# Optimization experiments

Hardware: AMD Instinct MI355X
Metric: run time of the kernel (lower is better)

Reference implementation:

```python
import jax, jax.numpy as jnp
import numpy as np

B = 131072
HIDDEN = [512, 512, 512, 512]
BETA = 20.0  # Softplus(beta=20)


def setup_inputs() -> dict:
    key = jax.random.key(0)
    dims = [3] + HIDDEN + [2]  # in_dim=3, out = div_mat_dim + 1 = 2
    n_layers = len(dims) - 1
    ks = jax.random.split(key, 1 + 2 * n_layers)
    d = {"tx": jax.random.normal(ks[0], (B, 3), dtype=jnp.float32)}
    for i, (din, dout) in enumerate(zip(dims[:-1], dims[1:])):
        lim = 1.0 / np.sqrt(din)  # torch nn.Linear default init
        d[f"W{i}"] = jax.random.uniform(ks[1 + 2 * i], (dout, din), jnp.float32, -lim, lim)
        d[f"b{i}"] = jax.random.uniform(ks[2 + 2 * i], (dout,), jnp.float32, -lim, lim)
    return d


def reference(tx, W0, b0, W1, b1, W2, b2, W3, b3, W4, b4):
    params = [(W0, b0), (W1, b1), (W2, b2), (W3, b3), (W4, b4)]

    def mlp(x):
        h = x
        for W, b in params[:-1]:
            # torch Softplus(beta=20): softplus(beta*x)/beta
            h = jax.nn.softplus(BETA * (h @ W.T + b)) / BETA
        W, b = params[-1]
        return h @ W.T + b  # [..., 2]: (stream fn s, pressure p)

    # div_A_matrix builds the 2x2 antisymmetric matrix A with A[0,1]=s, A[1,0]=-s.
    # vmap(jacrev(div_A_matrix)) then einsum('...ii') over the spatial cols (x,y)
    # reduces exactly to u = (ds/dy, -ds/dx). Per-sample grads of s are obtained
    # with one vectorized backward pass (samples are independent).
    g = jax.grad(lambda t: mlp(t)[:, 0].sum())(tx)  # [B, 3] cols = (t, x, y)
    u = jnp.stack([g[:, 2], -g[:, 1]], axis=1)      # [B, 2]
    p = mlp(tx)[:, -1:]                              # [B, 1]
    # torch .squeeze(0) is a no-op for B > 1
    return jnp.concatenate([u, p], axis=1)           # [B, 3]
```

## Files before the change

### kernel.cpp

```cpp
#include <hip/hip_runtime.h>

typedef _Float16 f16;
typedef __attribute__((ext_vector_type(8))) _Float16 f16x8;
typedef __attribute__((ext_vector_type(4))) float f32x4;

#define BT   131072
#define DD   512
#define TM   32
#define NBLK (BT / TM)

__device__ __forceinline__ void stA(char* tb, int row, int colbyte, float v) {
    *(f16*)(tb + row * 1024 + (colbyte ^ ((row & 7) << 4))) = (f16)v;
}
__device__ __forceinline__ f16x8 ldA8(const char* tb, int row, int kbyte) {
    return *(const f16x8*)(tb + row * 1024 + (kbyte ^ ((row & 7) << 4)));
}
__device__ __forceinline__ float ldh(const char* tb, int row, int colbyte) {
    return (float)*(const f16*)(tb + row * 1024 + (colbyte ^ ((row & 7) << 4)));
}

__device__ __forceinline__ f16x8 cvt8(const float* q) {
    float4 u0 = *(const float4*)q;
    float4 u1 = *(const float4*)(q + 4);
    f16x8 r;
    r[0] = (f16)u0.x; r[1] = (f16)u0.y; r[2] = (f16)u0.z; r[3] = (f16)u0.w;
    r[4] = (f16)u1.x; r[5] = (f16)u1.y; r[6] = (f16)u1.z; r[7] = (f16)u1.w;
    return r;
}

__global__ void prep_w(const float* __restrict__ W1, const float* __restrict__ W2,
                       const float* __restrict__ W3, f16* __restrict__ wp) {
    int tid = blockIdx.x * 256 + threadIdx.x;
    if (tid >= 6 * 16 * 32 * 64) return;
    int lane = tid & 63;
    int frag = tid >> 6;
    int nsub = frag & 31;
    int sk   = (frag >> 5) & 15;
    int l    = frag >> 9;
    int lw   = l - (l >= 3 ? 3 : 0);
    const float* W = (lw == 0) ? W1 : (lw == 1) ? W2 : W3;
    int n = nsub * 16 + (lane & 15);
    int k = sk * 32 + (lane >> 4) * 8;
    f16x8 o;
    if (l < 3) {
        const float* p = W + (size_t)n * DD + k;
        #pragma unroll
        for (int j = 0; j < 8; ++j) o[j] = (f16)p[j];
    } else {
        const float* p = W + (size_t)k * DD + n;
        #pragma unroll
        for (int j = 0; j < 8; ++j) o[j] = (f16)p[j * DD];
    }
    ((f16x8*)wp)[tid] = o;
}

#define MFMA1(A, B, C) __builtin_amdgcn_mfma_f32_16x16x32_f16(A, B, C, 0, 0, 0)

#define MFMA_SK2(TB, skc, Q0, Q1, Q2, Q3)                                      \
    { f16x8 aA = ldA8(TB, l15,      (skc) * 64 + g16 * 16);                    \
      f16x8 aB = ldA8(TB, 16 + l15, (skc) * 64 + g16 * 16);                    \
      acc[0][0] = MFMA1(aA, Q0, acc[0][0]); acc[0][1] = MFMA1(aA, Q1, acc[0][1]); \
      acc[0][2] = MFMA1(aA, Q2, acc[0][2]); acc[0][3] = MFMA1(aA, Q3, acc[0][3]); \
      acc[1][0] = MFMA1(aB, Q0, acc[1][0]); acc[1][1] = MFMA1(aB, Q1, acc[1][1]); \
      acc[1][2] = MFMA1(aB, Q2, acc[1][2]); acc[1][3] = MFMA1(aB, Q3, acc[1][3]); }

#define LOADB_P(wS, Q0, Q1, Q2, Q3, skc)                                       \
    { const f16x8* p_ = (wS) + ((size_t)(skc) << 11);                          \
      Q0 = p_[0]; Q1 = p_[64]; Q2 = p_[128]; Q3 = p_[192]; }

template<bool PREP>
__global__ __launch_bounds__(512) void mlp_fused(
    const float* __restrict__ tx,
    const float* __restrict__ W0, const float* __restrict__ b0v,
    const float* __restrict__ W1, const float* __restrict__ b1v,
    const float* __restrict__ W2, const float* __restrict__ b2v,
    const float* __restrict__ W3, const float* __restrict__ b3v,
    const float* __restrict__ W4, const float* __restrict__ b4v,
    const f16* __restrict__ wp, float* __restrict__ out)
{
    __shared__ __align__(16) short abuf_s[4 * 32 * DD];
    __shared__ float txb[TM * 3];
    __shared__ float pbuf[8][32];
    char* ab = (char*)abuf_s;
    char* G  = ab + 3 * 32768;

    const int tid  = threadIdx.x;
    const int lane = tid & 63;
    const int wv   = tid >> 6;
    const int g16  = lane >> 4;
    const int l15  = lane & 15;
    const long s0  = (long)blockIdx.x * TM;

    if (tid < TM * 3) txb[tid] = tx[s0 * 3 + tid];
    __syncthreads();

    {
        int n = tid;
        float w0 = W0[n * 3 + 0], w1 = W0[n * 3 + 1], w2 = W0[n * 3 + 2], bb = b0v[n];
        #pragma unroll 4
        for (int s = 0; s < TM; ++s) {
            float z  = fmaf(w0, txb[s * 3], fmaf(w1, txb[s * 3 + 1], fmaf(w2, txb[s * 3 + 2], bb)));
            float aa = fabsf(z);
            float e  = __expf(-20.f * aa);
            float dd = 1.f + e;
            float h  = fmaxf(z, 0.f) + __logf(dd) * 0.05f;
            stA(ab, s, n * 2, h);
        }
    }
    __syncthreads();

    for (int i = 0; i < 3; ++i) {
        const float* Wl = (i == 0) ? W1 : (i == 1) ? W2 : W3;
        const float* bl = (i == 0) ? b1v : (i == 1) ? b2v : b3v;
        const f16x8* wS = (const f16x8*)wp + (size_t)i * (16 * 32 * 64)
                        + (size_t)(wv * 4) * 64 + lane;
        const char* Tin = ab + i * 32768;

        f32x4 acc[2][4];
        #pragma unroll
        for (int m = 0; m < 2; ++m)
            #pragma unroll
            for (int n = 0; n < 4; ++n)
                acc[m][n] = f32x4{0.f, 0.f, 0.f, 0.f};

        #pragma unroll 2
        for (int sk = 0; sk < 16; ++sk) {
            f16x8 b0, b1, b2, b3;
            if constexpr (PREP) {
                LOADB_P(wS, b0, b1, b2, b3, sk)
            } else {
                const float* q = Wl + (size_t)(wv * 64 + l15) * DD + sk * 32 + g16 * 8;
                b0 = cvt8(q);
                b1 = cvt8(q + 16 * DD);
                b2 = cvt8(q + 32 * DD);
                b3 = cvt8(q + 48 * DD);
            }
            MFMA_SK2(Tin, sk, b0, b1, b2, b3)
        }

        if (i < 2) {
            char* Tout = ab + (i + 1) * 32768;
            #pragma unroll
            for (int m = 0; m < 2; ++m)
                #pragma unroll
                for (int n = 0; n < 4; ++n) {
                    float bias = bl[wv * 64 + n * 16 + l15];
                    int   cb   = (wv * 64 + n * 16 + l15) * 2;
                    #pragma unroll
                    for (int r = 0; r < 4; ++r) {
                        int row = m * 16 + g16 * 4 + r;
                        float z  = acc[m][n][r] + bias;
                        float aa = fabsf(z);
                        float e  = __expf(-20.f * aa);
                        float dd = 1.f + e;
                        float h  = fmaxf(z, 0.f) + __logf(dd) * 0.05f;
                        stA(Tout, row, cb, h);
                    }
                }
        } else {
            #pragma unroll
            for (int m = 0; m < 2; ++m)
                #pragma unroll
                for (int r = 0; r < 4; ++r) {
                    int row = m * 16 + g16 * 4 + r;
                    float pp = 0.f;
                    #pragma unroll
                    for (int n = 0; n < 4; ++n) {
                        int col = wv * 64 + n * 16 + l15;
                        float z  = acc[m][n][r] + bl[col];
                        float aa = fabsf(z);
                        float e  = __expf(-20.f * aa);
                        float dd = 1.f + e;
                        float rd = __builtin_amdgcn_rcpf(dd);
                        float h4 = fmaxf(z, 0.f) + __logf(dd) * 0.05f;
                        float sg = (z > 0.f ? 1.f : e) * rd;
                        pp = fmaf(W4[DD + col], h4, pp);
                        stA(G, row, col * 2, W4[col] * sg);
                    }
                    pp += __shfl_xor(pp, 1);
                    pp += __shfl_xor(pp, 2);
                    pp += __shfl_xor(pp, 4);
                    pp += __shfl_xor(pp, 8);
                    if (l15 == 0) pbuf[wv][row] = pp;
                }
        }
        __syncthreads();
    }

    for (int b = 0; b < 3; ++b) {
        const f16x8* wS = (const f16x8*)wp + (size_t)(5 - b) * (16 * 32 * 64)
                        + (size_t)(wv * 4) * 64 + lane;
        const float* Wb = (b == 0) ? W3 : (b == 1) ? W2 : W1;
        const char* Th = ab + (2 - b) * 32768;

        f32x4 acc[2][4];
        #pragma unroll
        for (int m = 0; m < 2; ++m)
            #pragma unroll
            for (int n = 0; n < 4; ++n)
                acc[m][n] = f32x4{0.f, 0.f, 0.f, 0.f};

        #pragma unroll 2
        for (int sk = 0; sk < 16; ++sk) {
            f16x8 b0, b1, b2, b3;
            if constexpr (PREP) {
                LOADB_P(wS, b0, b1, b2, b3, sk)
            } else {
                const float* q = Wb + (size_t)(sk * 32 + g16 * 8) * DD + wv * 64 + l15;
                f16x8 t0, t1, t2, t3;
                #pragma unroll
                for (int j = 0; j < 8; ++j) {
                    t0[j] = (f16)q[j * DD];
                    t1[j] = (f16)q[j * DD + 16];
                    t2[j] = (f16)q[j * DD + 32];
                    t3[j] = (f16)q[j * DD + 48];
                }
                b0 = t0; b1 = t1; b2 = t2; b3 = t3;
            }
            MFMA_SK2(G, sk, b0, b1, b2, b3)
        }
        __syncthreads();

        #pragma unroll
        for (int m = 0; m < 2; ++m)
            #pragma unroll
            for (int n = 0; n < 4; ++n) {
                int cb = (wv * 64 + n * 16 + l15) * 2;
                #pragma unroll
                for (int r = 0; r < 4; ++r) {
                    int row = m * 16 + g16 * 4 + r;
                    float h  = ldh(Th, row, cb);
                    float sg = 1.f - __expf(-20.f * h);
                    stA(G, row, cb, sg * acc[m][n][r]);
                }
            }
        __syncthreads();
    }

    {
        const int kb = lane * 8;
        float wyr[8], wxr[8];
        #pragma unroll
        for (int j = 0; j < 8; ++j) {
            wyr[j] = W0[(kb + j) * 3 + 2];
            wxr[j] = W0[(kb + j) * 3 + 1];
        }
        float bp = b4v[1];
        #pragma unroll
        for (int ii = 0; ii < 4; ++ii) {
            int s = wv * 4 + ii;
            f16x8 gg = ldA8(G, s, lane * 16);
            float dy = 0.f, dx = 0.f;
            #pragma unroll
            for (int j = 0; j < 8; ++j) {
                dy = fmaf(wyr[j], (float)gg[j], dy);
                dx = fmaf(wxr[j], (float)gg[j], dx);
            }
            #pragma unroll
            for (int mk = 1; mk < 64; mk <<= 1) {
                dy += __shfl_xor(dy, mk);
                dx += __shfl_xor(dx, mk);
            }
            if (lane == 0) {
                float ps = bp;
                #pragma unroll
                for (int w = 0; w < 8; ++w) ps += pbuf[w][s];
                float* o = out + (s0 + s) * 3;
                o[0] = dy;
                o[1] = -dx;
                o[2] = ps;
            }
        }
    }
}

extern "C" void kernel_launch(void* const* d_in, const int* in_sizes, int n_in,
                              void* d_out, int out_size, void* d_ws, size_t ws_size,
                              hipStream_t stream) {
    const float* tx = (const float*)d_in[0];
    const float* W0 = (const float*)d_in[1]; const float* b0 = (const float*)d_in[2];
    const float* W1 = (const float*)d_in[3]; const float* b1 = (const float*)d_in[4];
    const float* W2 = (const float*)d_in[5]; const float* b2 = (const float*)d_in[6];
    const float* W3 = (const float*)d_in[7]; const float* b3 = (const float*)d_in[8];
    const float* W4 = (const float*)d_in[9]; const float* b4 = (const float*)d_in[10];
    float* out = (float*)d_out;

    const size_t need = (size_t)6 * 512 * 512 * sizeof(f16);
    if (ws_size >= need) {
        f16* wp = (f16*)d_ws;
        prep_w<<<(6 * 16 * 32 * 64 + 255) / 256, 256, 0, stream>>>(W1, W2, W3, wp);
        mlp_fused<true><<<NBLK, 512, 0, stream>>>(tx, W0, b0, W1, b1, W2, b2, W3, b3, W4, b4, wp, out);
    } else {
        mlp_fused<false><<<NBLK, 512, 0, stream>>>(tx, W0, b0, W1, b1, W2, b2, W3, b3, W4, b4, nullptr, out);
    }
}
```

Before: 776.3 us.

## Double block size to 1024 threads, halving each wave's output column tile

Raises the workgroup from 8 to 16 waves. Each wave now computes 32 output columns instead of 64 in every forward and backward GEMM, and the layer-0 and final reduction loops are split across the extra waves. The goal is more latency hiding per CU and lower per-wave register pressure while keeping the same 32-sample tile and LDS footprint. The cost is twice as many A-tile LDS reads per unit of MFMA work, since A is reused across only two B fragments, plus more barrier participants.

```diff
diff --git a/kernel.cpp b/kernel.cpp
--- a/kernel.cpp
+++ b/kernel.cpp
@@ -56,20 +56,18 @@
 
 #define MFMA1(A, B, C) __builtin_amdgcn_mfma_f32_16x16x32_f16(A, B, C, 0, 0, 0)
 
-#define MFMA_SK2(TB, skc, Q0, Q1, Q2, Q3)                                      \
+#define MFMA_SK2(TB, skc, Q0, Q1)                                              \
     { f16x8 aA = ldA8(TB, l15,      (skc) * 64 + g16 * 16);                    \
       f16x8 aB = ldA8(TB, 16 + l15, (skc) * 64 + g16 * 16);                    \
       acc[0][0] = MFMA1(aA, Q0, acc[0][0]); acc[0][1] = MFMA1(aA, Q1, acc[0][1]); \
-      acc[0][2] = MFMA1(aA, Q2, acc[0][2]); acc[0][3] = MFMA1(aA, Q3, acc[0][3]); \
-      acc[1][0] = MFMA1(aB, Q0, acc[1][0]); acc[1][1] = MFMA1(aB, Q1, acc[1][1]); \
-      acc[1][2] = MFMA1(aB, Q2, acc[1][2]); acc[1][3] = MFMA1(aB, Q3, acc[1][3]); }
-
-#define LOADB_P(wS, Q0, Q1, Q2, Q3, skc)                                       \
+      acc[1][0] = MFMA1(aB, Q0, acc[1][0]); acc[1][1] = MFMA1(aB, Q1, acc[1][1]); }
+
+#define LOADB_P(wS, Q0, Q1, skc)                                               \
     { const f16x8* p_ = (wS) + ((size_t)(skc) << 11);                          \
-      Q0 = p_[0]; Q1 = p_[64]; Q2 = p_[128]; Q3 = p_[192]; }
+      Q0 = p_[0]; Q1 = p_[64]; }
 
 template<bool PREP>
-__global__ __launch_bounds__(512) void mlp_fused(
+__global__ __launch_bounds__(1024) void mlp_fused(
     const float* __restrict__ tx,
     const float* __restrict__ W0, const float* __restrict__ b0v,
     const float* __restrict__ W1, const float* __restrict__ b1v,
@@ -80,7 +78,7 @@
 {
     __shared__ __align__(16) short abuf_s[4 * 32 * DD];
     __shared__ float txb[TM * 3];
-    __shared__ float pbuf[8][32];
+    __shared__ float pbuf[16][32];
     char* ab = (char*)abuf_s;
     char* G  = ab + 3 * 32768;
 
@@ -95,10 +93,12 @@
     __syncthreads();
 
     {
-        int n = tid;
+        int n  = tid & 511;
+        int sb = (tid >> 9) * 16;
         float w0 = W0[n * 3 + 0], w1 = W0[n * 3 + 1], w2 = W0[n * 3 + 2], bb = b0v[n];
         #pragma unroll 4
-        for (int s = 0; s < TM; ++s) {
+        for (int si = 0; si < 16; ++si) {
+            int s = sb + si;
             float z  = fmaf(w0, txb[s * 3], fmaf(w1, txb[s * 3 + 1], fmaf(w2, txb[s * 3 + 2], bb)));
             float aa = fabsf(z);
             float e  = __expf(-20.f * aa);
@@ -113,29 +113,24 @@
         const float* Wl = (i == 0) ? W1 : (i == 1) ? W2 : W3;
         const float* bl = (i == 0) ? b1v : (i == 1) ? b2v : b3v;
         const f16x8* wS = (const f16x8*)wp + (size_t)i * (16 * 32 * 64)
-                        + (size_t)(wv * 4) * 64 + lane;
+                        + (size_t)(wv * 2) * 64 + lane;
         const char* Tin = ab + i * 32768;
 
-        f32x4 acc[2][4];
-        #pragma unroll
-        for (int m = 0; m < 2; ++m)
-            #pragma unroll
-            for (int n = 0; n < 4; ++n)
-                acc[m][n] = f32x4{0.f, 0.f, 0.f, 0.f};
+        f32x4 acc[2][2];
+        acc[0][0] = f32x4{0.f,0.f,0.f,0.f}; acc[0][1] = f32x4{0.f,0.f,0.f,0.f};
+        acc[1][0] = f32x4{0.f,0.f,0.f,0.f}; acc[1][1] = f32x4{0.f,0.f,0.f,0.f};
 
         #pragma unroll 2
         for (int sk = 0; sk < 16; ++sk) {
-            f16x8 b0, b1, b2, b3;
+            f16x8 b0, b1;
             if constexpr (PREP) {
-                LOADB_P(wS, b0, b1, b2, b3, sk)
+                LOADB_P(wS, b0, b1, sk)
             } else {
-                const float* q = Wl + (size_t)(wv * 64 + l15) * DD + sk * 32 + g16 * 8;
+                const float* q = Wl + (size_t)(wv * 32 + l15) * DD + sk * 32 + g16 * 8;
                 b0 = cvt8(q);
                 b1 = cvt8(q + 16 * DD);
-                b2 = cvt8(q + 32 * DD);
-                b3 = cvt8(q + 48 * DD);
-            }
-            MFMA_SK2(Tin, sk, b0, b1, b2, b3)
+            }
+            MFMA_SK2(Tin, sk, b0, b1)
         }
 
         if (i < 2) {
@@ -143,9 +138,9 @@
             #pragma unroll
             for (int m = 0; m < 2; ++m)
                 #pragma unroll
-                for (int n = 0; n < 4; ++n) {
-                    float bias = bl[wv * 64 + n * 16 + l15];
-                    int   cb   = (wv * 64 + n * 16 + l15) * 2;
+                for (int n = 0; n < 2; ++n) {
+                    float bias = bl[wv * 32 + n * 16 + l15];
+                    int   cb   = (wv * 32 + n * 16 + l15) * 2;
                     #pragma unroll
                     for (int r = 0; r < 4; ++r) {
                         int row = m * 16 + g16 * 4 + r;
@@ -165,8 +160,8 @@
                     int row = m * 16 + g16 * 4 + r;
                     float pp = 0.f;
                     #pragma unroll
-                    for (int n = 0; n < 4; ++n) {
-                        int col = wv * 64 + n * 16 + l15;
+                    for (int n = 0; n < 2; ++n) {
+                        int col = wv * 32 + n * 16 + l15;
                         float z  = acc[m][n][r] + bl[col];
                         float aa = fabsf(z);
                         float e  = __expf(-20.f * aa);
@@ -189,43 +184,38 @@
 
     for (int b = 0; b < 3; ++b) {
         const f16x8* wS = (const f16x8*)wp + (size_t)(5 - b) * (16 * 32 * 64)
-                        + (size_t)(wv * 4) * 64 + lane;
+                        + (size_t)(wv * 2) * 64 + lane;
         const float* Wb = (b == 0) ? W3 : (b == 1) ? W2 : W1;
         const char* Th = ab + (2 - b) * 32768;
 
-        f32x4 acc[2][4];
-        #pragma unroll
-        for (int m = 0; m < 2; ++m)
-            #pragma unroll
-            for (int n = 0; n < 4; ++n)
-                acc[m][n] = f32x4{0.f, 0.f, 0.f, 0.f};
+        f32x4 acc[2][2];
+        acc[0][0] = f32x4{0.f,0.f,0.f,0.f}; acc[0][1] = f32x4{0.f,0.f,0.f,0.f};
+        acc[1][0] = f32x4{0.f,0.f,0.f,0.f}; acc[1][1] = f32x4{0.f,0.f,0.f,0.f};
 
         #pragma unroll 2
         for (int sk = 0; sk < 16; ++sk) {
-            f16x8 b0, b1, b2, b3;
+            f16x8 b0, b1;
             if constexpr (PREP) {
-                LOADB_P(wS, b0, b1, b2, b3, sk)
+                LOADB_P(wS, b0, b1, sk)
             } else {
-                const float* q = Wb + (size_t)(sk * 32 + g16 * 8) * DD + wv * 64 + l15;
-                f16x8 t0, t1, t2, t3;
+                const float* q = Wb + (size_t)(sk * 32 + g16 * 8) * DD + wv * 32 + l15;
+                f16x8 t0, t1;
                 #pragma unroll
                 for (int j = 0; j < 8; ++j) {
                     t0[j] = (f16)q[j * DD];
                     t1[j] = (f16)q[j * DD + 16];
-                    t2[j] = (f16)q[j * DD + 32];
-                    t3[j] = (f16)q[j * DD + 48];
-                }
-                b0 = t0; b1 = t1; b2 = t2; b3 = t3;
-            }
-            MFMA_SK2(G, sk, b0, b1, b2, b3)
+                }
+                b0 = t0; b1 = t1;
+            }
+            MFMA_SK2(G, sk, b0, b1)
         }
         __syncthreads();
 
         #pragma unroll
         for (int m = 0; m < 2; ++m)
             #pragma unroll
-            for (int n = 0; n < 4; ++n) {
-                int cb = (wv * 64 + n * 16 + l15) * 2;
+            for (int n = 0; n < 2; ++n) {
+                int cb = (wv * 32 + n * 16 + l15) * 2;
                 #pragma unroll
                 for (int r = 0; r < 4; ++r) {
                     int row = m * 16 + g16 * 4 + r;
@@ -247,8 +237,8 @@
         }
         float bp = b4v[1];
         #pragma unroll
-        for (int ii = 0; ii < 4; ++ii) {
-            int s = wv * 4 + ii;
+        for (int ii = 0; ii < 2; ++ii) {
+            int s = wv * 2 + ii;
             f16x8 gg = ldA8(G, s, lane * 16);
             float dy = 0.f, dx = 0.f;
             #pragma unroll
@@ -264,7 +254,7 @@
             if (lane == 0) {
                 float ps = bp;
                 #pragma unroll
-                for (int w = 0; w < 8; ++w) ps += pbuf[w][s];
+                for (int w = 0; w < 16; ++w) ps += pbuf[w][s];
                 float* o = out + (s0 + s) * 3;
                 o[0] = dy;
                 o[1] = -dx;
@@ -289,8 +279,8 @@
     if (ws_size >= need) {
         f16* wp = (f16*)d_ws;
         prep_w<<<(6 * 16 * 32 * 64 + 255) / 256, 256, 0, stream>>>(W1, W2, W3, wp);
-        mlp_fused<true><<<NBLK, 512, 0, stream>>>(tx, W0, b0, W1, b1, W2, b2, W3, b3, W4, b4, wp, out);
+        mlp_fused<true><<<NBLK, 1024, 0, stream>>>(tx, W0, b0, W1, b1, W2, b2, W3, b3, W4, b4, wp, out);
     } else {
-        mlp_fused<false><<<NBLK, 512, 0, stream>>>(tx, W0, b0, W1, b1, W2, b2, W3, b3, W4, b4, nullptr, out);
-    }
-}
+        mlp_fused<false><<<NBLK, 1024, 0, stream>>>(tx, W0, b0, W1, b1, W2, b2, W3, b3, W4, b4, nullptr, out);
+    }
+}
```

After: 754.3 us. 2.8% less time.

## Process two 32-row sub-tiles per block to reuse weight loads

Applied to the files above, without the earlier changes.

Doubles the rows per block to 64 by running two 32-row sub-tiles that share each loaded weight fragment, so every B-operand load feeds twice as many MFMAs. The shared-memory plan changes from one buffer per layer to two ping-pong slots per sub-tile. The layer-1 softplus derivatives are kept in registers as f16, and the layer-0 derivative is recomputed from the inputs instead of being read back from stored activations. The cost is more accumulator and register pressure, which may lower occupancy, and half as many blocks in the grid.

```diff
diff --git a/kernel.cpp b/kernel.cpp
--- a/kernel.cpp
+++ b/kernel.cpp
@@ -6,8 +6,8 @@
 
 #define BT   131072
 #define DD   512
-#define TM   32
-#define NBLK (BT / TM)
+#define TMB  64
+#define NBLK (BT / TMB)
 
 __device__ __forceinline__ void stA(char* tb, int row, int colbyte, float v) {
     *(f16*)(tb + row * 1024 + (colbyte ^ ((row & 7) << 4))) = (f16)v;
@@ -56,17 +56,51 @@
 
 #define MFMA1(A, B, C) __builtin_amdgcn_mfma_f32_16x16x32_f16(A, B, C, 0, 0, 0)
 
-#define MFMA_SK2(TB, skc, Q0, Q1, Q2, Q3)                                      \
-    { f16x8 aA = ldA8(TB, l15,      (skc) * 64 + g16 * 16);                    \
-      f16x8 aB = ldA8(TB, 16 + l15, (skc) * 64 + g16 * 16);                    \
-      acc[0][0] = MFMA1(aA, Q0, acc[0][0]); acc[0][1] = MFMA1(aA, Q1, acc[0][1]); \
-      acc[0][2] = MFMA1(aA, Q2, acc[0][2]); acc[0][3] = MFMA1(aA, Q3, acc[0][3]); \
-      acc[1][0] = MFMA1(aB, Q0, acc[1][0]); acc[1][1] = MFMA1(aB, Q1, acc[1][1]); \
-      acc[1][2] = MFMA1(aB, Q2, acc[1][2]); acc[1][3] = MFMA1(aB, Q3, acc[1][3]); }
-
-#define LOADB_P(wS, Q0, Q1, Q2, Q3, skc)                                       \
-    { const f16x8* p_ = (wS) + ((size_t)(skc) << 11);                          \
-      Q0 = p_[0]; Q1 = p_[64]; Q2 = p_[128]; Q3 = p_[192]; }
+#define MFMA_TILE(ACC, SA, skc, Q0, Q1, Q2, Q3)                                \
+    { f16x8 a0_ = ldA8(SA, l15,      (skc) * 64 + g16 * 16);                   \
+      f16x8 a1_ = ldA8(SA, 16 + l15, (skc) * 64 + g16 * 16);                   \
+      ACC[0][0]=MFMA1(a0_,Q0,ACC[0][0]); ACC[0][1]=MFMA1(a0_,Q1,ACC[0][1]);    \
+      ACC[0][2]=MFMA1(a0_,Q2,ACC[0][2]); ACC[0][3]=MFMA1(a0_,Q3,ACC[0][3]);    \
+      ACC[1][0]=MFMA1(a1_,Q0,ACC[1][0]); ACC[1][1]=MFMA1(a1_,Q1,ACC[1][1]);    \
+      ACC[1][2]=MFMA1(a1_,Q2,ACC[1][2]); ACC[1][3]=MFMA1(a1_,Q3,ACC[1][3]); }
+
+#define ZACC(A)                                                                \
+    _Pragma("unroll") for (int m_ = 0; m_ < 2; ++m_)                           \
+    _Pragma("unroll") for (int n_ = 0; n_ < 4; ++n_)                           \
+        A[m_][n_] = f32x4{0.f, 0.f, 0.f, 0.f};
+
+#define KLOOP_P(SEC, SLOT)                                                     \
+  { const f16x8* wS = (const f16x8*)wp + (size_t)(SEC) * (16*32*64)            \
+                    + (size_t)(wv * 4) * 64 + lane;                            \
+    _Pragma("unroll 2")                                                        \
+    for (int sk = 0; sk < 16; ++sk) {                                          \
+      const f16x8* p_ = wS + ((size_t)sk << 11);                               \
+      f16x8 q0 = p_[0], q1 = p_[64], q2 = p_[128], q3 = p_[192];               \
+      MFMA_TILE(acc0, TA0 + (SLOT)*32768, sk, q0, q1, q2, q3)                  \
+      MFMA_TILE(acc1, TA1 + (SLOT)*32768, sk, q0, q1, q2, q3)                  \
+    } }
+
+#define KLOOP_FW(WPTR, SLOT)                                                   \
+  { _Pragma("unroll 2")                                                        \
+    for (int sk = 0; sk < 16; ++sk) {                                          \
+      const float* q_ = WPTR + (size_t)(wv*64 + l15)*DD + sk*32 + g16*8;       \
+      f16x8 q0 = cvt8(q_), q1 = cvt8(q_ + 16*DD);                              \
+      f16x8 q2 = cvt8(q_ + 32*DD), q3 = cvt8(q_ + 48*DD);                      \
+      MFMA_TILE(acc0, TA0 + (SLOT)*32768, sk, q0, q1, q2, q3)                  \
+      MFMA_TILE(acc1, TA1 + (SLOT)*32768, sk, q0, q1, q2, q3)                  \
+    } }
+
+#define KLOOP_BW(WPTR, SLOT)                                                   \
+  { for (int sk = 0; sk < 16; ++sk) {                                          \
+      const float* q_ = WPTR + (size_t)(sk*32 + g16*8)*DD + wv*64 + l15;       \
+      f16x8 t0, t1, t2, t3;                                                    \
+      _Pragma("unroll")                                                        \
+      for (int j = 0; j < 8; ++j) {                                            \
+          t0[j] = (f16)q_[j*DD];      t1[j] = (f16)q_[j*DD + 16];              \
+          t2[j] = (f16)q_[j*DD + 32]; t3[j] = (f16)q_[j*DD + 48]; }            \
+      MFMA_TILE(acc0, TA0 + (SLOT)*32768, sk, t0, t1, t2, t3)                  \
+      MFMA_TILE(acc1, TA1 + (SLOT)*32768, sk, t0, t1, t2, t3)                  \
+    } }
 
 template<bool PREP>
 __global__ __launch_bounds__(512) void mlp_fused(
@@ -79,163 +113,190 @@
     const f16* __restrict__ wp, float* __restrict__ out)
 {
     __shared__ __align__(16) short abuf_s[4 * 32 * DD];
-    __shared__ float txb[TM * 3];
-    __shared__ float pbuf[8][32];
-    char* ab = (char*)abuf_s;
-    char* G  = ab + 3 * 32768;
+    __shared__ float txb[TMB * 3];
+    __shared__ float pbuf[2][8][32];
+    char* ab  = (char*)abuf_s;
+    char* TA0 = ab;
+    char* TA1 = ab + 65536;
 
     const int tid  = threadIdx.x;
     const int lane = tid & 63;
     const int wv   = tid >> 6;
     const int g16  = lane >> 4;
     const int l15  = lane & 15;
-    const long s0  = (long)blockIdx.x * TM;
-
-    if (tid < TM * 3) txb[tid] = tx[s0 * 3 + tid];
+    const long s0g = (long)blockIdx.x * TMB;
+
+    if (tid < TMB * 3) txb[tid] = tx[s0g * 3 + tid];
     __syncthreads();
 
     {
         int n = tid;
-        float w0 = W0[n * 3 + 0], w1 = W0[n * 3 + 1], w2 = W0[n * 3 + 2], bb = b0v[n];
+        float w0 = W0[n*3], w1 = W0[n*3+1], w2 = W0[n*3+2], bb = b0v[n];
         #pragma unroll 4
-        for (int s = 0; s < TM; ++s) {
-            float z  = fmaf(w0, txb[s * 3], fmaf(w1, txb[s * 3 + 1], fmaf(w2, txb[s * 3 + 2], bb)));
+        for (int s = 0; s < TMB; ++s) {
+            float z  = fmaf(w0, txb[s*3], fmaf(w1, txb[s*3+1], fmaf(w2, txb[s*3+2], bb)));
             float aa = fabsf(z);
             float e  = __expf(-20.f * aa);
-            float dd = 1.f + e;
-            float h  = fmaxf(z, 0.f) + __logf(dd) * 0.05f;
-            stA(ab, s, n * 2, h);
+            float d2 = 1.f + e;
+            float h  = fmaxf(z, 0.f) + __logf(d2) * 0.05f;
+            stA(ab + (s >> 5) * 65536, s & 31, n * 2, h);
         }
     }
     __syncthreads();
 
-    for (int i = 0; i < 3; ++i) {
-        const float* Wl = (i == 0) ? W1 : (i == 1) ? W2 : W3;
-        const float* bl = (i == 0) ? b1v : (i == 1) ? b2v : b3v;
-        const f16x8* wS = (const f16x8*)wp + (size_t)i * (16 * 32 * 64)
-                        + (size_t)(wv * 4) * 64 + lane;
-        const char* Tin = ab + i * 32768;
-
-        f32x4 acc[2][4];
-        #pragma unroll
-        for (int m = 0; m < 2; ++m)
-            #pragma unroll
-            for (int n = 0; n < 4; ++n)
-                acc[m][n] = f32x4{0.f, 0.f, 0.f, 0.f};
-
-        #pragma unroll 2
-        for (int sk = 0; sk < 16; ++sk) {
-            f16x8 b0, b1, b2, b3;
-            if constexpr (PREP) {
-                LOADB_P(wS, b0, b1, b2, b3, sk)
-            } else {
-                const float* q = Wl + (size_t)(wv * 64 + l15) * DD + sk * 32 + g16 * 8;
-                b0 = cvt8(q);
-                b1 = cvt8(q + 16 * DD);
-                b2 = cvt8(q + 32 * DD);
-                b3 = cvt8(q + 48 * DD);
-            }
-            MFMA_SK2(Tin, sk, b0, b1, b2, b3)
+    f32x4 acc0[2][4], acc1[2][4];
+    f16x8 sg2a[4], sg2b[4];
+
+    ZACC(acc0) ZACC(acc1)
+    if constexpr (PREP) { KLOOP_P(0, 0) } else { KLOOP_FW(W1, 0) }
+    #pragma unroll
+    for (int n = 0; n < 4; ++n) {
+        float bias = b1v[wv*64 + n*16 + l15];
+        int   cb   = (wv*64 + n*16 + l15) * 2;
+        #pragma unroll
+        for (int m = 0; m < 2; ++m)
+            #pragma unroll
+            for (int r = 0; r < 4; ++r) {
+                int row = m*16 + g16*4 + r;
+                int idx = m*16 + n*4 + r;
+                { float z = acc0[m][n][r] + bias;
+                  float e = __expf(-20.f * fabsf(z));
+                  float d2 = 1.f + e;
+                  float h = fmaxf(z, 0.f) + __logf(d2) * 0.05f;
+                  sg2a[idx>>3][idx&7] = (f16)((z > 0.f ? 1.f : e) * __builtin_amdgcn_rcpf(d2));
+                  stA(TA0 + 32768, row, cb, h); }
+                { float z = acc1[m][n][r] + bias;
+                  float e = __expf(-20.f * fabsf(z));
+                  float d2 = 1.f + e;
+                  float h = fmaxf(z, 0.f) + __logf(d2) * 0.05f;
+                  sg2b[idx>>3][idx&7] = (f16)((z > 0.f ? 1.f : e) * __builtin_amdgcn_rcpf(d2));
+                  stA(TA1 + 32768, row, cb, h); }
+            }
+    }
+    __syncthreads();
+
+    ZACC(acc0) ZACC(acc1)
+    if constexpr (PREP) { KLOOP_P(1, 1) } else { KLOOP_FW(W2, 1) }
+    #pragma unroll
+    for (int n = 0; n < 4; ++n) {
+        float bias = b2v[wv*64 + n*16 + l15];
+        int   cb   = (wv*64 + n*16 + l15) * 2;
+        #pragma unroll
+        for (int m = 0; m < 2; ++m)
+            #pragma unroll
+            for (int r = 0; r < 4; ++r) {
+                int row = m*16 + g16*4 + r;
+                { float z = acc0[m][n][r] + bias;
+                  float e = __expf(-20.f * fabsf(z));
+                  float d2 = 1.f + e;
+                  stA(TA0, row, cb, fmaxf(z, 0.f) + __logf(d2) * 0.05f); }
+                { float z = acc1[m][n][r] + bias;
+                  float e = __expf(-20.f * fabsf(z));
+                  float d2 = 1.f + e;
+                  stA(TA1, row, cb, fmaxf(z, 0.f) + __logf(d2) * 0.05f); }
+            }
+    }
+    __syncthreads();
+
+    ZACC(acc0) ZACC(acc1)
+    if constexpr (PREP) { KLOOP_P(2, 0) } else { KLOOP_FW(W3, 0) }
+    #pragma unroll
+    for (int m = 0; m < 2; ++m)
+        #pragma unroll
+        for (int r = 0; r < 4; ++r) {
+            int row = m*16 + g16*4 + r;
+            float pp0 = 0.f, pp1 = 0.f;
+            #pragma unroll
+            for (int n = 0; n < 4; ++n) {
+                int col = wv*64 + n*16 + l15;
+                int cb  = col * 2;
+                float w4s = W4[col], w4p = W4[DD + col], bias = b3v[col];
+                { float z = acc0[m][n][r] + bias;
+                  float e = __expf(-20.f * fabsf(z));
+                  float d2 = 1.f + e;
+                  float rd = __builtin_amdgcn_rcpf(d2);
+                  float h4 = fmaxf(z, 0.f) + __logf(d2) * 0.05f;
+                  float sg = (z > 0.f ? 1.f : e) * rd;
+                  pp0 = fmaf(w4p, h4, pp0);
+                  stA(TA0 + 32768, row, cb, w4s * sg); }
+                { float z = acc1[m][n][r] + bias;
+                  float e = __expf(-20.f * fabsf(z));
+                  float d2 = 1.f + e;
+                  float rd = __builtin_amdgcn_rcpf(d2);
+                  float h4 = fmaxf(z, 0.f) + __logf(d2) * 0.05f;
+                  float sg = (z > 0.f ? 1.f : e) * rd;
+                  pp1 = fmaf(w4p, h4, pp1);
+                  stA(TA1 + 32768, row, cb, w4s * sg); }
+            }
+            pp0 += __shfl_xor(pp0, 1); pp0 += __shfl_xor(pp0, 2);
+            pp0 += __shfl_xor(pp0, 4); pp0 += __shfl_xor(pp0, 8);
+            pp1 += __shfl_xor(pp1, 1); pp1 += __shfl_xor(pp1, 2);
+            pp1 += __shfl_xor(pp1, 4); pp1 += __shfl_xor(pp1, 8);
+            if (l15 == 0) { pbuf[0][wv][row] = pp0; pbuf[1][wv][row] = pp1; }
         }
-
-        if (i < 2) {
-            char* Tout = ab + (i + 1) * 32768;
-            #pragma unroll
-            for (int m = 0; m < 2; ++m)
-                #pragma unroll
-                for (int n = 0; n < 4; ++n) {
-                    float bias = bl[wv * 64 + n * 16 + l15];
-                    int   cb   = (wv * 64 + n * 16 + l15) * 2;
-                    #pragma unroll
-                    for (int r = 0; r < 4; ++r) {
-                        int row = m * 16 + g16 * 4 + r;
-                        float z  = acc[m][n][r] + bias;
-                        float aa = fabsf(z);
-                        float e  = __expf(-20.f * aa);
-                        float dd = 1.f + e;
-                        float h  = fmaxf(z, 0.f) + __logf(dd) * 0.05f;
-                        stA(Tout, row, cb, h);
-                    }
-                }
-        } else {
-            #pragma unroll
-            for (int m = 0; m < 2; ++m)
-                #pragma unroll
-                for (int r = 0; r < 4; ++r) {
-                    int row = m * 16 + g16 * 4 + r;
-                    float pp = 0.f;
-                    #pragma unroll
-                    for (int n = 0; n < 4; ++n) {
-                        int col = wv * 64 + n * 16 + l15;
-                        float z  = acc[m][n][r] + bl[col];
-                        float aa = fabsf(z);
-                        float e  = __expf(-20.f * aa);
-                        float dd = 1.f + e;
-                        float rd = __builtin_amdgcn_rcpf(dd);
-                        float h4 = fmaxf(z, 0.f) + __logf(dd) * 0.05f;
-                        float sg = (z > 0.f ? 1.f : e) * rd;
-                        pp = fmaf(W4[DD + col], h4, pp);
-                        stA(G, row, col * 2, W4[col] * sg);
-                    }
-                    pp += __shfl_xor(pp, 1);
-                    pp += __shfl_xor(pp, 2);
-                    pp += __shfl_xor(pp, 4);
-                    pp += __shfl_xor(pp, 8);
-                    if (l15 == 0) pbuf[wv][row] = pp;
-                }
-        }
-        __syncthreads();
-    }
-
-    for (int b = 0; b < 3; ++b) {
-        const f16x8* wS = (const f16x8*)wp + (size_t)(5 - b) * (16 * 32 * 64)
-                        + (size_t)(wv * 4) * 64 + lane;
-        const float* Wb = (b == 0) ? W3 : (b == 1) ? W2 : W1;
-        const char* Th = ab + (2 - b) * 32768;
-
-        f32x4 acc[2][4];
-        #pragma unroll
-        for (int m = 0; m < 2; ++m)
-            #pragma unroll
-            for (int n = 0; n < 4; ++n)
-                acc[m][n] = f32x4{0.f, 0.f, 0.f, 0.f};
-
-        #pragma unroll 2
-        for (int sk = 0; sk < 16; ++sk) {
-            f16x8 b0, b1, b2, b3;
-            if constexpr (PREP) {
-                LOADB_P(wS, b0, b1, b2, b3, sk)
-            } else {
-                const float* q = Wb + (size_t)(sk * 32 + g16 * 8) * DD + wv * 64 + l15;
-                f16x8 t0, t1, t2, t3;
-                #pragma unroll
-                for (int j = 0; j < 8; ++j) {
-                    t0[j] = (f16)q[j * DD];
-                    t1[j] = (f16)q[j * DD + 16];
-                    t2[j] = (f16)q[j * DD + 32];
-                    t3[j] = (f16)q[j * DD + 48];
-                }
-                b0 = t0; b1 = t1; b2 = t2; b3 = t3;
-            }
-            MFMA_SK2(G, sk, b0, b1, b2, b3)
-        }
-        __syncthreads();
-
-        #pragma unroll
-        for (int m = 0; m < 2; ++m)
-            #pragma unroll
-            for (int n = 0; n < 4; ++n) {
-                int cb = (wv * 64 + n * 16 + l15) * 2;
-                #pragma unroll
-                for (int r = 0; r < 4; ++r) {
-                    int row = m * 16 + g16 * 4 + r;
-                    float h  = ldh(Th, row, cb);
-                    float sg = 1.f - __expf(-20.f * h);
-                    stA(G, row, cb, sg * acc[m][n][r]);
-                }
-            }
-        __syncthreads();
-    }
+    __syncthreads();
+
+    ZACC(acc0) ZACC(acc1)
+    if constexpr (PREP) { KLOOP_P(5, 1) } else { KLOOP_BW(W3, 1) }
+    #pragma unroll
+    for (int n = 0; n < 4; ++n) {
+        int cb = (wv*64 + n*16 + l15) * 2;
+        #pragma unroll
+        for (int m = 0; m < 2; ++m)
+            #pragma unroll
+            for (int r = 0; r < 4; ++r) {
+                int row = m*16 + g16*4 + r;
+                { float h3 = ldh(TA0, row, cb);
+                  float sg = 1.f - __expf(-20.f * h3);
+                  stA(TA0, row, cb, sg * acc0[m][n][r]); }
+                { float h3 = ldh(TA1, row, cb);
+                  float sg = 1.f - __expf(-20.f * h3);
+                  stA(TA1, row, cb, sg * acc1[m][n][r]); }
+            }
+    }
+    __syncthreads();
+
+    ZACC(acc0) ZACC(acc1)
+    if constexpr (PREP) { KLOOP_P(4, 0) } else { KLOOP_BW(W2, 0) }
+    #pragma unroll
+    for (int n = 0; n < 4; ++n) {
+        int cb = (wv*64 + n*16 + l15) * 2;
+        #pragma unroll
+        for (int m = 0; m < 2; ++m)
+            #pragma unroll
+            for (int r = 0; r < 4; ++r) {
+                int row = m*16 + g16*4 + r;
+                int idx = m*16 + n*4 + r;
+                stA(TA0 + 32768, row, cb, (float)sg2a[idx>>3][idx&7] * acc0[m][n][r]);
+                stA(TA1 + 32768, row, cb, (float)sg2b[idx>>3][idx&7] * acc1[m][n][r]);
+            }
+    }
+    __syncthreads();
+
+    ZACC(acc0) ZACC(acc1)
+    if constexpr (PREP) { KLOOP_P(3, 1) } else { KLOOP_BW(W1, 1) }
+    #pragma unroll
+    for (int n = 0; n < 4; ++n) {
+        int col = wv*64 + n*16 + l15;
+        int cb  = col * 2;
+        float w00 = W0[col*3], w01 = W0[col*3+1], w02 = W0[col*3+2], bb = b0v[col];
+        #pragma unroll
+        for (int m = 0; m < 2; ++m)
+            #pragma unroll
+            for (int r = 0; r < 4; ++r) {
+                int row = m*16 + g16*4 + r;
+                { float z = fmaf(w00, txb[row*3], fmaf(w01, txb[row*3+1], fmaf(w02, txb[row*3+2], bb)));
+                  float e = __expf(-20.f * fabsf(z));
+                  float sg = (z > 0.f ? 1.f : e) * __builtin_amdgcn_rcpf(1.f + e);
+                  stA(TA0, row, cb, sg * acc0[m][n][r]); }
+                { int s = 32 + row;
+                  float z = fmaf(w00, txb[s*3], fmaf(w01, txb[s*3+1], fmaf(w02, txb[s*3+2], bb)));
+                  float e = __expf(-20.f * fabsf(z));
+                  float sg = (z > 0.f ? 1.f : e) * __builtin_amdgcn_rcpf(1.f + e);
+                  stA(TA1, row, cb, sg * acc1[m][n][r]); }
+            }
+    }
+    __syncthreads();
 
     {
         const int kb = lane * 8;
@@ -247,9 +308,11 @@
         }
         float bp = b4v[1];
         #pragma unroll
-        for (int ii = 0; ii < 4; ++ii) {
-            int s = wv * 4 + ii;
-            f16x8 gg = ldA8(G, s, lane * 16);
+        for (int ii = 0; ii < 8; ++ii) {
+            int s   = wv * 8 + ii;
+            int row = s & 31;
+            const char* Gt = ab + (s >> 5) * 65536;
+            f16x8 gg = ldA8(Gt, row, lane * 16);
             float dy = 0.f, dx = 0.f;
             #pragma unroll
             for (int j = 0; j < 8; ++j) {
@@ -264,8 +327,8 @@
             if (lane == 0) {
                 float ps = bp;
                 #pragma unroll
-                for (int w = 0; w < 8; ++w) ps += pbuf[w][s];
-                float* o = out + (s0 + s) * 3;
+                for (int w = 0; w < 8; ++w) ps += pbuf[s >> 5][w][row];
+                float* o = out + (s0g + s) * 3;
                 o[0] = dy;
                 o[1] = -dx;
                 o[2] = ps;
```

Result: slower. 1.112 ms (+43.3%).
